# Kernel tuning notes

Hardware: AMD Instinct MI355X
Metric: run time of the kernel (lower is better)

The kernel has to match this reference:

```python
import jax, jax.numpy as jnp
import numpy as np

K, D = 1024, 256
B, H, W = 16, 64, 64


def setup_inputs() -> dict:
    key = jax.random.key(0)
    k1, k2 = jax.random.split(key)
    z_e_x = jax.random.normal(k1, (B, D, H, W), dtype=jnp.float32)
    # nn.Embedding weight initialized uniform(-1/K, 1/K)
    embedding = jax.random.uniform(k2, (K, D), dtype=jnp.float32,
                                   minval=-1.0 / K, maxval=1.0 / K)
    return {"z_e_x": z_e_x, "embedding": embedding}


def reference(z_e_x, embedding):
    # permute(0,2,3,1): [B,D,H,W] -> [B,H,W,D]
    z = jnp.transpose(z_e_x, (0, 2, 3, 1))
    flat = z.reshape(-1, z.shape[-1])  # [N, D], N = B*H*W
    # squared L2 distances: ||z||^2 - 2 z.e + ||e||^2  -> [N, K]
    dists = (jnp.sum(flat * flat, axis=1, keepdims=True)
             - 2.0 * flat @ embedding.T
             + jnp.sum(embedding * embedding, axis=1))
    indices = jnp.argmin(dists, axis=1)  # [N]
    # vq() returns latents with the spatial shape [B, H, W]
    return indices.reshape(z.shape[:-1]).astype(jnp.int32)
```

## Files before the change

kernel.cpp:

```cpp
#include <hip/hip_runtime.h>


#define D_DIM  256
#define K_DIM  1024
#define HW     4096
#define N_TOT  65536
#define NSPLIT 4
#define KSPL   (K_DIM / NSPLIT)
#define KT     64
#define NKT    (KSPL / KT)
#define F32MAX 3.402823466e38f


__global__ void ee_kernel(const float* __restrict__ e, float* __restrict__ ee) {
#pragma clang fp contract(off)
    int k = blockIdx.x * blockDim.x + threadIdx.x;
    if (k >= K_DIM) return;
    const float* row = e + (size_t)k * D_DIM;
    float total = 0.0f;
    #pragma unroll
    for (int h = 0; h < 2; ++h) {
        const float* a = row + h * 128;
        float r[8];
        #pragma unroll
        for (int j = 0; j < 8; ++j) { float v = a[j]; r[j] = v * v; }
        #pragma unroll
        for (int i = 8; i < 128; i += 8) {
            #pragma unroll
            for (int j = 0; j < 8; ++j) { float v = a[i + j]; r[j] = r[j] + v * v; }
        }
        float s = ((r[0] + r[1]) + (r[2] + r[3])) + ((r[4] + r[5]) + (r[6] + r[7]));
        total = (h == 0) ? s : (total + s);
    }
    ee[k] = total;
}

__global__ void a_kernel(const float* __restrict__ z, float* __restrict__ A) {
#pragma clang fp contract(off)
    int n = blockIdx.x * blockDim.x + threadIdx.x;
    int b  = n >> 12;
    int hw = n & (HW - 1);
    const float* base = z + (size_t)b * D_DIM * HW + hw;
    float total = 0.0f;
    #pragma unroll
    for (int h = 0; h < 2; ++h) {
        float r[8];
        #pragma unroll
        for (int j = 0; j < 8; ++j) {
            float v = base[(size_t)(h * 128 + j) * HW];
            r[j] = v * v;
        }
        #pragma unroll
        for (int i = 8; i < 128; i += 8) {
            #pragma unroll
            for (int j = 0; j < 8; ++j) {
                float v = base[(size_t)(h * 128 + i + j) * HW];
                r[j] = r[j] + v * v;
            }
        }
        float s = ((r[0] + r[1]) + (r[2] + r[3])) + ((r[4] + r[5]) + (r[6] + r[7]));
        total = (h == 0) ? s : (total + s);
    }
    A[n] = total;
}


__global__ void et_kernel(const float* __restrict__ e, float* __restrict__ eT) {
    int k = blockIdx.x;
    int d = threadIdx.x;
    eT[(size_t)d * K_DIM + k] = 2.0f * e[(size_t)k * D_DIM + d];
}


__launch_bounds__(256, 4)
__global__ void vq_partial(const float* __restrict__ z, const float* __restrict__ eT,
                           const float* __restrict__ A, const float* __restrict__ ee,
                           float* __restrict__ pv, int* __restrict__ pk) {
#pragma clang fp contract(off)
    const int tid  = threadIdx.x;
    const int s    = blockIdx.x & (NSPLIT - 1);
    const int slab = blockIdx.x >> 2;
    const int n    = slab * 256 + tid;
    const int b    = n >> 12;
    const int hw   = n & (HW - 1);
    const float* __restrict__ zp = z + (size_t)b * D_DIM * HW + hw;
    const int kb0 = s * KSPL;

    const float An = A[n];
    float bestv = F32MAX;
    int   bestk = 0;

    float za[8], zb[8];
    #pragma unroll
    for (int i = 0; i < 8; ++i) za[i] = zp[(size_t)i * HW];

    #pragma unroll 1
    for (int kt = 0; kt < NKT; ++kt) {
        const int kbase = kb0 + kt * KT;
        float acc[KT];
        #pragma unroll
        for (int j = 0; j < KT; ++j) acc[j] = 0.0f;

        #pragma unroll 1
        for (int it = 0; it < 16; ++it) {
            const int base = it * 16;
            #pragma unroll
            for (int i = 0; i < 8; ++i)
                zb[i] = zp[(size_t)((base + 8 + i) & (D_DIM - 1)) * HW];
            #pragma unroll
            for (int dd = 0; dd < 8; ++dd) {
                const float zv = za[dd];
                const float* __restrict__ er = eT + (size_t)(base + dd) * K_DIM + kbase;
                #pragma unroll
                for (int j = 0; j < KT; ++j)
                    acc[j] = fmaf(zv, er[j], acc[j]);
            }
            #pragma unroll
            for (int i = 0; i < 8; ++i)
                za[i] = zp[(size_t)((base + 16 + i) & (D_DIM - 1)) * HW];
            #pragma unroll
            for (int dd = 0; dd < 8; ++dd) {
                const float zv = zb[dd];
                const float* __restrict__ er = eT + (size_t)(base + 8 + dd) * K_DIM + kbase;
                #pragma unroll
                for (int j = 0; j < KT; ++j)
                    acc[j] = fmaf(zv, er[j], acc[j]);
            }
        }

        #pragma unroll
        for (int j = 0; j < KT; ++j) {
            const float dist = (An - acc[j]) + ee[kbase + j];
            if (dist < bestv) { bestv = dist; bestk = kbase + j; }
        }
    }

    pv[(size_t)s * N_TOT + n] = bestv;
    pk[(size_t)s * N_TOT + n] = bestk;
}


__global__ void combine_kernel(const float* __restrict__ pv, const int* __restrict__ pk,
                               int* __restrict__ out) {
    int n = blockIdx.x * blockDim.x + threadIdx.x;
    float bv = pv[n];
    int   bk = pk[n];
    #pragma unroll
    for (int s2 = 1; s2 < NSPLIT; ++s2) {
        float v = pv[(size_t)s2 * N_TOT + n];
        int   k = pk[(size_t)s2 * N_TOT + n];
        if (v < bv) { bv = v; bk = k; }
    }
    out[n] = bk;
}

extern "C" void kernel_launch(void* const* d_in, const int* in_sizes, int n_in,
                              void* d_out, int out_size, void* d_ws, size_t ws_size,
                              hipStream_t stream) {
    const float* z   = (const float*)d_in[0];
    const float* emb = (const float*)d_in[1];
    int* out = (int*)d_out;

    float* wsA  = (float*)d_ws;
    float* wsEE = wsA + N_TOT;
    float* wsET = wsEE + K_DIM;
    float* wsPV = wsET + (size_t)D_DIM * K_DIM;
    int*   wsPK = (int*)(wsPV + (size_t)NSPLIT * N_TOT);

    et_kernel<<<K_DIM, 256, 0, stream>>>(emb, wsET);
    ee_kernel<<<K_DIM / 256, 256, 0, stream>>>(emb, wsEE);
    a_kernel<<<N_TOT / 256, 256, 0, stream>>>(z, wsA);
    vq_partial<<<N_TOT / 256 * NSPLIT, 256, 0, stream>>>(z, wsET, wsA, wsEE, wsPV, wsPK);
    combine_kernel<<<N_TOT / 256, 256, 0, stream>>>(wsPV, wsPK, out);
}
```

Before: 511.9 us.

## Register-block two rows per thread and pack codebook into contiguous tiles

```diff
diff --git a/kernel.cpp b/kernel.cpp
--- a/kernel.cpp
+++ b/kernel.cpp
@@ -5,9 +5,9 @@
 #define K_DIM  1024
 #define HW     4096
 #define N_TOT  65536
-#define NSPLIT 4
+#define NSPLIT 8
 #define KSPL   (K_DIM / NSPLIT)
-#define KT     64
+#define KT     32
 #define NKT    (KSPL / KT)
 #define F32MAX 3.402823466e38f
 
@@ -65,78 +65,105 @@
 }
 
 
-__global__ void et_kernel(const float* __restrict__ e, float* __restrict__ eT) {
+__global__ void pack_kernel(const float* __restrict__ e, float* __restrict__ epk) {
     int k = blockIdx.x;
     int d = threadIdx.x;
-    eT[(size_t)d * K_DIM + k] = 2.0f * e[(size_t)k * D_DIM + d];
+    int s  = k >> 7;
+    int kt = (k >> 5) & (NKT - 1);
+    int j  = k & (KT - 1);
+    epk[(((size_t)(s * NKT + kt) * D_DIM + d) * KT) + j] = 2.0f * e[(size_t)k * D_DIM + d];
 }
 
 
 __launch_bounds__(256, 4)
-__global__ void vq_partial(const float* __restrict__ z, const float* __restrict__ eT,
+__global__ void vq_partial(const float* __restrict__ z, const float* __restrict__ epk,
                            const float* __restrict__ A, const float* __restrict__ ee,
                            float* __restrict__ pv, int* __restrict__ pk) {
 #pragma clang fp contract(off)
     const int tid  = threadIdx.x;
     const int s    = blockIdx.x & (NSPLIT - 1);
-    const int slab = blockIdx.x >> 2;
-    const int n    = slab * 256 + tid;
-    const int b    = n >> 12;
-    const int hw   = n & (HW - 1);
-    const float* __restrict__ zp = z + (size_t)b * D_DIM * HW + hw;
-    const int kb0 = s * KSPL;
-
-    const float An = A[n];
-    float bestv = F32MAX;
-    int   bestk = 0;
-
-    float za[8], zb[8];
-    #pragma unroll
-    for (int i = 0; i < 8; ++i) za[i] = zp[(size_t)i * HW];
+    const int slab = blockIdx.x >> 3;
+    const int n0   = slab * 512 + tid;
+    const int n1   = n0 + 256;
+    const int b    = n0 >> 12;
+    const float* __restrict__ zp0 = z + (size_t)b * D_DIM * HW + (n0 & (HW - 1));
+    const float* __restrict__ zp1 = z + (size_t)b * D_DIM * HW + (n1 & (HW - 1));
+    const float* __restrict__ ebase = epk + (size_t)s * (NKT * D_DIM * KT);
+
+    const float An0 = A[n0];
+    const float An1 = A[n1];
+    float best0 = F32MAX, best1 = F32MAX;
+    int   bk0 = 0, bk1 = 0;
+
+    float za0[8], za1[8], zb0[8], zb1[8];
+    #pragma unroll
+    for (int i = 0; i < 8; ++i) {
+        za0[i] = zp0[(size_t)i * HW];
+        za1[i] = zp1[(size_t)i * HW];
+    }
 
     #pragma unroll 1
     for (int kt = 0; kt < NKT; ++kt) {
-        const int kbase = kb0 + kt * KT;
-        float acc[KT];
-        #pragma unroll
-        for (int j = 0; j < KT; ++j) acc[j] = 0.0f;
+        const float* __restrict__ ek = ebase + (size_t)kt * (D_DIM * KT);
+        float a0[KT], a1[KT];
+        #pragma unroll
+        for (int j = 0; j < KT; ++j) { a0[j] = 0.0f; a1[j] = 0.0f; }
 
         #pragma unroll 1
         for (int it = 0; it < 16; ++it) {
             const int base = it * 16;
             #pragma unroll
-            for (int i = 0; i < 8; ++i)
-                zb[i] = zp[(size_t)((base + 8 + i) & (D_DIM - 1)) * HW];
+            for (int i = 0; i < 8; ++i) {
+                const size_t idx = (size_t)((base + 8 + i) & (D_DIM - 1)) * HW;
+                zb0[i] = zp0[idx];
+                zb1[i] = zp1[idx];
+            }
             #pragma unroll
             for (int dd = 0; dd < 8; ++dd) {
-                const float zv = za[dd];
-                const float* __restrict__ er = eT + (size_t)(base + dd) * K_DIM + kbase;
+                const float zv0 = za0[dd], zv1 = za1[dd];
+                const float* __restrict__ er = ek + (size_t)(base + dd) * KT;
                 #pragma unroll
-                for (int j = 0; j < KT; ++j)
-                    acc[j] = fmaf(zv, er[j], acc[j]);
-            }
-            #pragma unroll
-            for (int i = 0; i < 8; ++i)
-                za[i] = zp[(size_t)((base + 16 + i) & (D_DIM - 1)) * HW];
+                for (int j = 0; j < KT; ++j) {
+                    const float ev = er[j];
+                    a0[j] = fmaf(zv0, ev, a0[j]);
+                    a1[j] = fmaf(zv1, ev, a1[j]);
+                }
+            }
+            #pragma unroll
+            for (int i = 0; i < 8; ++i) {
+                const size_t idx = (size_t)((base + 16 + i) & (D_DIM - 1)) * HW;
+                za0[i] = zp0[idx];
+                za1[i] = zp1[idx];
+            }
             #pragma unroll
             for (int dd = 0; dd < 8; ++dd) {
-                const float zv = zb[dd];
-                const float* __restrict__ er = eT + (size_t)(base + 8 + dd) * K_DIM + kbase;
+                const float zv0 = zb0[dd], zv1 = zb1[dd];
+                const float* __restrict__ er = ek + (size_t)(base + 8 + dd) * KT;
                 #pragma unroll
-                for (int j = 0; j < KT; ++j)
-                    acc[j] = fmaf(zv, er[j], acc[j]);
-            }
-        }
-
+                for (int j = 0; j < KT; ++j) {
+                    const float ev = er[j];
+                    a0[j] = fmaf(zv0, ev, a0[j]);
+                    a1[j] = fmaf(zv1, ev, a1[j]);
+                }
+            }
+        }
+
+        const int kbase = s * KSPL + kt * KT;
         #pragma unroll
         for (int j = 0; j < KT; ++j) {
-            const float dist = (An - acc[j]) + ee[kbase + j];
-            if (dist < bestv) { bestv = dist; bestk = kbase + j; }
-        }
-    }
-
-    pv[(size_t)s * N_TOT + n] = bestv;
-    pk[(size_t)s * N_TOT + n] = bestk;
+            const int kg = kbase + j;
+            const float eev = ee[kg];
+            const float d0 = (An0 - a0[j]) + eev;
+            const float d1 = (An1 - a1[j]) + eev;
+            if (d0 < best0) { best0 = d0; bk0 = kg; }
+            if (d1 < best1) { best1 = d1; bk1 = kg; }
+        }
+    }
+
+    pv[(size_t)s * N_TOT + n0] = best0;
+    pk[(size_t)s * N_TOT + n0] = bk0;
+    pv[(size_t)s * N_TOT + n1] = best1;
+    pk[(size_t)s * N_TOT + n1] = bk1;
 }
 
 
@@ -161,15 +188,15 @@
     const float* emb = (const float*)d_in[1];
     int* out = (int*)d_out;
 
-    float* wsA  = (float*)d_ws;
-    float* wsEE = wsA + N_TOT;
-    float* wsET = wsEE + K_DIM;
-    float* wsPV = wsET + (size_t)D_DIM * K_DIM;
-    int*   wsPK = (int*)(wsPV + (size_t)NSPLIT * N_TOT);
-
-    et_kernel<<<K_DIM, 256, 0, stream>>>(emb, wsET);
+    float* wsA   = (float*)d_ws;
+    float* wsEE  = wsA + N_TOT;
+    float* wsEPK = wsEE + K_DIM;
+    float* wsPV  = wsEPK + (size_t)D_DIM * K_DIM;
+    int*   wsPK  = (int*)(wsPV + (size_t)NSPLIT * N_TOT);
+
+    pack_kernel<<<K_DIM, 256, 0, stream>>>(emb, wsEPK);
     ee_kernel<<<K_DIM / 256, 256, 0, stream>>>(emb, wsEE);
     a_kernel<<<N_TOT / 256, 256, 0, stream>>>(z, wsA);
-    vq_partial<<<N_TOT / 256 * NSPLIT, 256, 0, stream>>>(z, wsET, wsA, wsEE, wsPV, wsPK);
+    vq_partial<<<(N_TOT / 512) * NSPLIT, 256, 0, stream>>>(z, wsEPK, wsA, wsEE, wsPV, wsPK);
     combine_kernel<<<N_TOT / 256, 256, 0, stream>>>(wsPV, wsPK, out);
 }
```

Result: no change. 518.9 us (+1.4%).

## Stage z tile in LDS, pack codebook in 16-wide tiles, combine splits in-block

Applied to the files above, without the earlier changes.

```diff
diff --git a/kernel.cpp b/kernel.cpp
--- a/kernel.cpp
+++ b/kernel.cpp
@@ -5,10 +5,11 @@
 #define K_DIM  1024
 #define HW     4096
 #define N_TOT  65536
-#define NSPLIT 4
-#define KSPL   (K_DIM / NSPLIT)
-#define KT     64
-#define NKT    (KSPL / KT)
+#define KT     16
+#define NLB    64
+#define KSP    4
+#define KRANGE (K_DIM / KSP)
+#define NPASS  (KRANGE / KT)
 #define F32MAX 3.402823466e38f
 
 
@@ -65,93 +66,122 @@
 }
 
 
-__global__ void et_kernel(const float* __restrict__ e, float* __restrict__ eT) {
+__global__ void pack_kernel(const float* __restrict__ e, float* __restrict__ epk) {
     int k = blockIdx.x;
     int d = threadIdx.x;
-    eT[(size_t)d * K_DIM + k] = 2.0f * e[(size_t)k * D_DIM + d];
-}
-
-
-__launch_bounds__(256, 4)
-__global__ void vq_partial(const float* __restrict__ z, const float* __restrict__ eT,
-                           const float* __restrict__ A, const float* __restrict__ ee,
-                           float* __restrict__ pv, int* __restrict__ pk) {
+    epk[((size_t)(k >> 4) * D_DIM + d) * KT + (k & 15)] = 2.0f * e[(size_t)k * D_DIM + d];
+}
+
+
+__launch_bounds__(256, 2)
+__global__ void vq_main(const float* __restrict__ z, const float* __restrict__ epk,
+                        const float* __restrict__ A, const float* __restrict__ ee,
+                        int* __restrict__ out) {
 #pragma clang fp contract(off)
-    const int tid  = threadIdx.x;
-    const int s    = blockIdx.x & (NSPLIT - 1);
-    const int slab = blockIdx.x >> 2;
-    const int n    = slab * 256 + tid;
-    const int b    = n >> 12;
-    const int hw   = n & (HW - 1);
-    const float* __restrict__ zp = z + (size_t)b * D_DIM * HW + hw;
-    const int kb0 = s * KSPL;
-
-    const float An = A[n];
+    __shared__ __align__(16) unsigned char smem[D_DIM * NLB * 4];
+    float* zs = (float*)smem;
+
+    const int tid = threadIdx.x;
+    const int nl  = tid & (NLB - 1);
+    const int ks  = tid >> 6;
+    const int n0  = blockIdx.x * NLB;
+    const int b   = n0 >> 12;
+    const int hw0 = n0 & (HW - 1);
+    const float* __restrict__ zbase = z + (size_t)b * D_DIM * HW + hw0;
+
+    #pragma unroll
+    for (int rep = 0; rep < 16; ++rep) {
+        int fidx = rep * 256 + tid;
+        int d  = fidx >> 4;
+        int n4 = (fidx & 15) * 4;
+        float4 v = *(const float4*)(zbase + (size_t)d * HW + n4);
+        *(float4*)&zs[d * NLB + n4] = v;
+    }
+    __syncthreads();
+
+    int lz;
+    asm volatile("v_mov_b32 %0, 0" : "=v"(lz));
+    const float* __restrict__ eb = epk + (size_t)ks * (NPASS * D_DIM * KT) + lz;
+
+    const float An = A[n0 + nl];
     float bestv = F32MAX;
     int   bestk = 0;
 
-    float za[8], zb[8];
-    #pragma unroll
-    for (int i = 0; i < 8; ++i) za[i] = zp[(size_t)i * HW];
-
     #pragma unroll 1
-    for (int kt = 0; kt < NKT; ++kt) {
-        const int kbase = kb0 + kt * KT;
+    for (int p = 0; p < NPASS; ++p) {
+        const float* __restrict__ ep = eb + (size_t)p * (D_DIM * KT);
         float acc[KT];
         #pragma unroll
         for (int j = 0; j < KT; ++j) acc[j] = 0.0f;
 
+        float4 ebuf[4][4];
+        float  zbuf[4];
+        #pragma unroll
+        for (int s = 0; s < 4; ++s) {
+            const float4* e4 = (const float4*)(ep + s * KT);
+            ebuf[s][0] = e4[0]; ebuf[s][1] = e4[1];
+            ebuf[s][2] = e4[2]; ebuf[s][3] = e4[3];
+            zbuf[s] = zs[s * NLB + nl];
+        }
+
         #pragma unroll 1
-        for (int it = 0; it < 16; ++it) {
-            const int base = it * 16;
+        for (int dd = 0; dd < D_DIM; dd += 4) {
+            const bool pf = (dd + 4 < D_DIM);
             #pragma unroll
-            for (int i = 0; i < 8; ++i)
-                zb[i] = zp[(size_t)((base + 8 + i) & (D_DIM - 1)) * HW];
-            #pragma unroll
-            for (int dd = 0; dd < 8; ++dd) {
-                const float zv = za[dd];
-                const float* __restrict__ er = eT + (size_t)(base + dd) * K_DIM + kbase;
-                #pragma unroll
-                for (int j = 0; j < KT; ++j)
-                    acc[j] = fmaf(zv, er[j], acc[j]);
+            for (int s = 0; s < 4; ++s) {
+                const float zv = zbuf[s];
+                const float4 e0 = ebuf[s][0], e1 = ebuf[s][1];
+                const float4 e2 = ebuf[s][2], e3 = ebuf[s][3];
+                acc[ 0] = fmaf(zv, e0.x, acc[ 0]);
+                acc[ 1] = fmaf(zv, e0.y, acc[ 1]);
+                acc[ 2] = fmaf(zv, e0.z, acc[ 2]);
+                acc[ 3] = fmaf(zv, e0.w, acc[ 3]);
+                acc[ 4] = fmaf(zv, e1.x, acc[ 4]);
+                acc[ 5] = fmaf(zv, e1.y, acc[ 5]);
+                acc[ 6] = fmaf(zv, e1.z, acc[ 6]);
+                acc[ 7] = fmaf(zv, e1.w, acc[ 7]);
+                acc[ 8] = fmaf(zv, e2.x, acc[ 8]);
+                acc[ 9] = fmaf(zv, e2.y, acc[ 9]);
+                acc[10] = fmaf(zv, e2.z, acc[10]);
+                acc[11] = fmaf(zv, e2.w, acc[11]);
+                acc[12] = fmaf(zv, e3.x, acc[12]);
+                acc[13] = fmaf(zv, e3.y, acc[13]);
+                acc[14] = fmaf(zv, e3.z, acc[14]);
+                acc[15] = fmaf(zv, e3.w, acc[15]);
+                if (pf) {
+                    const float4* e4 = (const float4*)(ep + (dd + 4 + s) * KT);
+                    ebuf[s][0] = e4[0]; ebuf[s][1] = e4[1];
+                    ebuf[s][2] = e4[2]; ebuf[s][3] = e4[3];
+                    zbuf[s] = zs[(dd + 4 + s) * NLB + nl];
+                }
             }
-            #pragma unroll
-            for (int i = 0; i < 8; ++i)
-                za[i] = zp[(size_t)((base + 16 + i) & (D_DIM - 1)) * HW];
-            #pragma unroll
-            for (int dd = 0; dd < 8; ++dd) {
-                const float zv = zb[dd];
-                const float* __restrict__ er = eT + (size_t)(base + 8 + dd) * K_DIM + kbase;
-                #pragma unroll
-                for (int j = 0; j < KT; ++j)
-                    acc[j] = fmaf(zv, er[j], acc[j]);
-            }
-        }
-
+        }
+
+        const int kb = ks * KRANGE + p * KT;
         #pragma unroll
         for (int j = 0; j < KT; ++j) {
-            const float dist = (An - acc[j]) + ee[kbase + j];
-            if (dist < bestv) { bestv = dist; bestk = kbase + j; }
-        }
-    }
-
-    pv[(size_t)s * N_TOT + n] = bestv;
-    pk[(size_t)s * N_TOT + n] = bestk;
-}
-
-
-__global__ void combine_kernel(const float* __restrict__ pv, const int* __restrict__ pk,
-                               int* __restrict__ out) {
-    int n = blockIdx.x * blockDim.x + threadIdx.x;
-    float bv = pv[n];
-    int   bk = pk[n];
-    #pragma unroll
-    for (int s2 = 1; s2 < NSPLIT; ++s2) {
-        float v = pv[(size_t)s2 * N_TOT + n];
-        int   k = pk[(size_t)s2 * N_TOT + n];
-        if (v < bv) { bv = v; bk = k; }
-    }
-    out[n] = bk;
+            const float dist = (An - acc[j]) + ee[kb + j];
+            if (dist < bestv) { bestv = dist; bestk = kb + j; }
+        }
+    }
+
+    __syncthreads();
+    float* cv = (float*)smem;
+    int*   ck = (int*)(smem + KSP * NLB * 4);
+    cv[ks * NLB + nl] = bestv;
+    ck[ks * NLB + nl] = bestk;
+    __syncthreads();
+    if (ks == 0) {
+        float bv = cv[nl];
+        int   bk = ck[nl];
+        #pragma unroll
+        for (int s2 = 1; s2 < KSP; ++s2) {
+            float v = cv[s2 * NLB + nl];
+            int   k = ck[s2 * NLB + nl];
+            if (v < bv) { bv = v; bk = k; }
+        }
+        out[n0 + nl] = bk;
+    }
 }
 
 extern "C" void kernel_launch(void* const* d_in, const int* in_sizes, int n_in,
@@ -161,15 +191,12 @@
     const float* emb = (const float*)d_in[1];
     int* out = (int*)d_out;
 
-    float* wsA  = (float*)d_ws;
-    float* wsEE = wsA + N_TOT;
-    float* wsET = wsEE + K_DIM;
-    float* wsPV = wsET + (size_t)D_DIM * K_DIM;
-    int*   wsPK = (int*)(wsPV + (size_t)NSPLIT * N_TOT);
-
-    et_kernel<<<K_DIM, 256, 0, stream>>>(emb, wsET);
+    float* wsA   = (float*)d_ws;
+    float* wsEE  = wsA + N_TOT;
+    float* wsEPK = wsEE + K_DIM;
+
+    pack_kernel<<<K_DIM, 256, 0, stream>>>(emb, wsEPK);
     ee_kernel<<<K_DIM / 256, 256, 0, stream>>>(emb, wsEE);
     a_kernel<<<N_TOT / 256, 256, 0, stream>>>(z, wsA);
-    vq_partial<<<N_TOT / 256 * NSPLIT, 256, 0, stream>>>(z, wsET, wsA, wsEE, wsPV, wsPK);
-    combine_kernel<<<N_TOT / 256, 256, 0, stream>>>(wsPV, wsPK, out);
-}
+    vq_main<<<N_TOT / NLB, 256, 0, stream>>>(z, wsEPK, wsA, wsEE, out);
+}
```

Result: slower. 2.021 ms (+294.9%).

## Fuse prep kernels, split K eightfold, and combine results with packed atomicMin

Applied to the files above, without the earlier changes.

```diff
diff --git a/kernel.cpp b/kernel.cpp
--- a/kernel.cpp
+++ b/kernel.cpp
@@ -5,98 +5,104 @@
 #define K_DIM  1024
 #define HW     4096
 #define N_TOT  65536
-#define NSPLIT 4
+#define NSPLIT 8
 #define KSPL   (K_DIM / NSPLIT)
 #define KT     64
 #define NKT    (KSPL / KT)
 #define F32MAX 3.402823466e38f
 
 
-__global__ void ee_kernel(const float* __restrict__ e, float* __restrict__ ee) {
+__global__ void prep_kernel(const float* __restrict__ e, const float* __restrict__ z,
+                            float* __restrict__ epk, float* __restrict__ ee,
+                            float* __restrict__ A, unsigned long long* __restrict__ packed) {
 #pragma clang fp contract(off)
-    int k = blockIdx.x * blockDim.x + threadIdx.x;
-    if (k >= K_DIM) return;
-    const float* row = e + (size_t)k * D_DIM;
-    float total = 0.0f;
-    #pragma unroll
-    for (int h = 0; h < 2; ++h) {
-        const float* a = row + h * 128;
-        float r[8];
+    const int bid = blockIdx.x;
+    const int tid = threadIdx.x;
+
+    if (bid < 1024) {
+        const int k = bid, d = tid;
+        const int g = k >> 6, j = k & 63;
+        epk[((size_t)g * D_DIM + d) * KT + j] = 2.0f * e[(size_t)k * D_DIM + d];
+        return;
+    }
+    if (bid < 1028) {
+        const int k = (bid - 1024) * 256 + tid;
+        const float* row = e + (size_t)k * D_DIM;
+        float total = 0.0f;
         #pragma unroll
-        for (int j = 0; j < 8; ++j) { float v = a[j]; r[j] = v * v; }
+        for (int h = 0; h < 2; ++h) {
+            const float* a = row + h * 128;
+            float r[8];
+            #pragma unroll
+            for (int j = 0; j < 8; ++j) { float v = a[j]; r[j] = v * v; }
+            #pragma unroll
+            for (int i = 8; i < 128; i += 8) {
+                #pragma unroll
+                for (int j = 0; j < 8; ++j) { float v = a[i + j]; r[j] = r[j] + v * v; }
+            }
+            float s = ((r[0] + r[1]) + (r[2] + r[3])) + ((r[4] + r[5]) + (r[6] + r[7]));
+            total = (h == 0) ? s : (total + s);
+        }
+        ee[k] = total;
+        return;
+    }
+    {
+        const int n = (bid - 1028) * 256 + tid;
+        const int b  = n >> 12;
+        const int hw = n & (HW - 1);
+        const float* base = z + (size_t)b * D_DIM * HW + hw;
+        float total = 0.0f;
         #pragma unroll
-        for (int i = 8; i < 128; i += 8) {
-            #pragma unroll
-            for (int j = 0; j < 8; ++j) { float v = a[i + j]; r[j] = r[j] + v * v; }
-        }
-        float s = ((r[0] + r[1]) + (r[2] + r[3])) + ((r[4] + r[5]) + (r[6] + r[7]));
-        total = (h == 0) ? s : (total + s);
-    }
-    ee[k] = total;
-}
-
-__global__ void a_kernel(const float* __restrict__ z, float* __restrict__ A) {
-#pragma clang fp contract(off)
-    int n = blockIdx.x * blockDim.x + threadIdx.x;
-    int b  = n >> 12;
-    int hw = n & (HW - 1);
-    const float* base = z + (size_t)b * D_DIM * HW + hw;
-    float total = 0.0f;
-    #pragma unroll
-    for (int h = 0; h < 2; ++h) {
-        float r[8];
-        #pragma unroll
-        for (int j = 0; j < 8; ++j) {
-            float v = base[(size_t)(h * 128 + j) * HW];
-            r[j] = v * v;
-        }
-        #pragma unroll
-        for (int i = 8; i < 128; i += 8) {
+        for (int h = 0; h < 2; ++h) {
+            float r[8];
             #pragma unroll
             for (int j = 0; j < 8; ++j) {
-                float v = base[(size_t)(h * 128 + i + j) * HW];
-                r[j] = r[j] + v * v;
+                float v = base[(size_t)(h * 128 + j) * HW];
+                r[j] = v * v;
             }
+            #pragma unroll
+            for (int i = 8; i < 128; i += 8) {
+                #pragma unroll
+                for (int j = 0; j < 8; ++j) {
+                    float v = base[(size_t)(h * 128 + i + j) * HW];
+                    r[j] = r[j] + v * v;
+                }
+            }
+            float s = ((r[0] + r[1]) + (r[2] + r[3])) + ((r[4] + r[5]) + (r[6] + r[7]));
+            total = (h == 0) ? s : (total + s);
         }
-        float s = ((r[0] + r[1]) + (r[2] + r[3])) + ((r[4] + r[5]) + (r[6] + r[7]));
-        total = (h == 0) ? s : (total + s);
+        A[n] = total;
+        packed[n] = ~0ULL;
     }
-    A[n] = total;
 }
 
 
-__global__ void et_kernel(const float* __restrict__ e, float* __restrict__ eT) {
-    int k = blockIdx.x;
-    int d = threadIdx.x;
-    eT[(size_t)d * K_DIM + k] = 2.0f * e[(size_t)k * D_DIM + d];
-}
-
-
-__launch_bounds__(256, 4)
-__global__ void vq_partial(const float* __restrict__ z, const float* __restrict__ eT,
+__launch_bounds__(256, 5)
+__global__ void vq_partial(const float* __restrict__ z, const float* __restrict__ epk,
                            const float* __restrict__ A, const float* __restrict__ ee,
-                           float* __restrict__ pv, int* __restrict__ pk) {
+                           unsigned long long* __restrict__ packed) {
 #pragma clang fp contract(off)
     const int tid  = threadIdx.x;
     const int s    = blockIdx.x & (NSPLIT - 1);
-    const int slab = blockIdx.x >> 2;
+    const int slab = blockIdx.x >> 3;
     const int n    = slab * 256 + tid;
     const int b    = n >> 12;
-    const int hw   = n & (HW - 1);
-    const float* __restrict__ zp = z + (size_t)b * D_DIM * HW + hw;
-    const int kb0 = s * KSPL;
+    const float* __restrict__ zp = z + (size_t)b * D_DIM * HW + (n & (HW - 1));
+    const int w = __builtin_amdgcn_readfirstlane(tid) >> 6;
 
     const float An = A[n];
-    float bestv = F32MAX;
-    int   bestk = 0;
+    unsigned long long best = ~0ULL;
 
     float za[8], zb[8];
     #pragma unroll
     for (int i = 0; i < 8; ++i) za[i] = zp[(size_t)i * HW];
 
     #pragma unroll 1
-    for (int kt = 0; kt < NKT; ++kt) {
-        const int kbase = kb0 + kt * KT;
+    for (int t = 0; t < NKT; ++t) {
+        const int kt = t ^ (w & 1);
+        const int g  = 2 * s + kt;
+        const float* __restrict__ ep = epk + (size_t)g * (D_DIM * KT);
+
         float acc[KT];
         #pragma unroll
         for (int j = 0; j < KT; ++j) acc[j] = 0.0f;
@@ -110,7 +116,7 @@
             #pragma unroll
             for (int dd = 0; dd < 8; ++dd) {
                 const float zv = za[dd];
-                const float* __restrict__ er = eT + (size_t)(base + dd) * K_DIM + kbase;
+                const float* __restrict__ er = ep + (size_t)(base + dd) * KT;
                 #pragma unroll
                 for (int j = 0; j < KT; ++j)
                     acc[j] = fmaf(zv, er[j], acc[j]);
@@ -121,37 +127,30 @@
             #pragma unroll
             for (int dd = 0; dd < 8; ++dd) {
                 const float zv = zb[dd];
-                const float* __restrict__ er = eT + (size_t)(base + 8 + dd) * K_DIM + kbase;
+                const float* __restrict__ er = ep + (size_t)(base + 8 + dd) * KT;
                 #pragma unroll
                 for (int j = 0; j < KT; ++j)
                     acc[j] = fmaf(zv, er[j], acc[j]);
             }
         }
 
+        const int kb = s * KSPL + kt * KT;
         #pragma unroll
         for (int j = 0; j < KT; ++j) {
-            const float dist = (An - acc[j]) + ee[kbase + j];
-            if (dist < bestv) { bestv = dist; bestk = kbase + j; }
+            const float dist = (An - acc[j]) + ee[kb + j];
+            const unsigned long long p =
+                ((unsigned long long)__float_as_uint(dist) << 32) | (unsigned)(kb + j);
+            if (p < best) best = p;
         }
     }
 
-    pv[(size_t)s * N_TOT + n] = bestv;
-    pk[(size_t)s * N_TOT + n] = bestk;
+    atomicMin(&packed[n], best);
 }
 
-
-__global__ void combine_kernel(const float* __restrict__ pv, const int* __restrict__ pk,
-                               int* __restrict__ out) {
-    int n = blockIdx.x * blockDim.x + threadIdx.x;
-    float bv = pv[n];
-    int   bk = pk[n];
-    #pragma unroll
-    for (int s2 = 1; s2 < NSPLIT; ++s2) {
-        float v = pv[(size_t)s2 * N_TOT + n];
-        int   k = pk[(size_t)s2 * N_TOT + n];
-        if (v < bv) { bv = v; bk = k; }
-    }
-    out[n] = bk;
+__global__ void fin_kernel(const unsigned long long* __restrict__ packed,
+                           int* __restrict__ out) {
+    const int n = blockIdx.x * 256 + threadIdx.x;
+    out[n] = (int)(unsigned)(packed[n] & 0xffffffffULL);
 }
 
 extern "C" void kernel_launch(void* const* d_in, const int* in_sizes, int n_in,
@@ -161,15 +160,12 @@
     const float* emb = (const float*)d_in[1];
     int* out = (int*)d_out;
 
-    float* wsA  = (float*)d_ws;
-    float* wsEE = wsA + N_TOT;
-    float* wsET = wsEE + K_DIM;
-    float* wsPV = wsET + (size_t)D_DIM * K_DIM;
-    int*   wsPK = (int*)(wsPV + (size_t)NSPLIT * N_TOT);
+    unsigned long long* wsP = (unsigned long long*)d_ws;
+    float* wsA   = (float*)(wsP + N_TOT);
+    float* wsEE  = wsA + N_TOT;
+    float* wsEPK = wsEE + K_DIM;
 
-    et_kernel<<<K_DIM, 256, 0, stream>>>(emb, wsET);
-    ee_kernel<<<K_DIM / 256, 256, 0, stream>>>(emb, wsEE);
-    a_kernel<<<N_TOT / 256, 256, 0, stream>>>(z, wsA);
-    vq_partial<<<N_TOT / 256 * NSPLIT, 256, 0, stream>>>(z, wsET, wsA, wsEE, wsPV, wsPK);
-    combine_kernel<<<N_TOT / 256, 256, 0, stream>>>(wsPV, wsPK, out);
+    prep_kernel<<<1284, 256, 0, stream>>>(emb, z, wsEPK, wsEE, wsA, wsP);
+    vq_partial<<<(N_TOT / 256) * NSPLIT, 256, 0, stream>>>(z, wsEPK, wsA, wsEE, wsP);
+    fin_kernel<<<N_TOT / 256, 256, 0, stream>>>(wsP, out);
 }
```

New measurement: 1.337 ms. +161.3%, slower.
